# Kernel tuning notes

Hardware: AMD Instinct MI355X
Metric: run time of the kernel (lower is better)

Reference implementation:

```python
import jax, jax.numpy as jnp
import numpy as np

NQ = 100000   # query-side nodes (len of `input`)
NKV = 100000  # key/value-side nodes (len of `other`)
E = 2000000   # edges
D = 64        # n_embed
H = 4         # n_heads
F = D // H    # head dim


def setup_inputs() -> dict:
    key = jax.random.key(0)
    ks = jax.random.split(key, 8)
    sc = 1.0 / np.sqrt(D).astype(np.float32)
    inp = jax.random.normal(ks[0], (NQ, D), jnp.float32)
    oth = jax.random.normal(ks[1], (NKV, D), jnp.float32)
    t = jax.random.randint(ks[2], (E,), 0, NQ, jnp.int32)
    s = jax.random.randint(ks[3], (E,), 0, NKV, jnp.int32)
    Wq = jax.random.normal(ks[4], (D, D), jnp.float32) * sc    # p_q weight (applied as x @ Wq)
    Wkv = jax.random.normal(ks[5], (D, 2 * D), jnp.float32) * sc  # p_kv weight
    Wo = jax.random.normal(ks[6], (D, D), jnp.float32) * sc    # out weight
    bo = jax.random.normal(ks[7], (D,), jnp.float32) * sc      # out bias
    return {"input": inp, "other": oth, "t": t, "s": s,
            "Wq": Wq, "Wkv": Wkv, "Wo": Wo, "bo": bo}


def reference(input, other, t, s, Wq, Wkv, Wo, bo):
    # projections: q [NQ,H,F], k/v [NKV,H,F]
    q = (input @ Wq).reshape(NQ, H, F)
    kv = other @ Wkv
    k = kv[:, :D].reshape(NKV, H, F)
    v = kv[:, D:].reshape(NKV, H, F)

    # per-edge attention scores: [E, H]
    score = jnp.einsum('ehf,ehf->eh', q[t], k[s]) / jnp.sqrt(jnp.float32(F))

    # scatter-softmax over edges grouped by target node t (dim_size = NQ)
    smax = jax.ops.segment_max(score, t, num_segments=NQ)          # [NQ, H]
    smax = jnp.where(jnp.isfinite(smax), smax, jnp.float32(0.0))   # empty segments
    ex = jnp.exp(score - smax[t])                                  # [E, H]
    ssum = jax.ops.segment_sum(ex, t, num_segments=NQ)             # [NQ, H]
    alpha = ex / ssum[t]                                           # [E, H]

    # scatter-sum of weighted values: [NQ, H, F]
    out = jax.ops.segment_sum(alpha[..., None] * v[s], t, num_segments=NQ)
    return out.reshape(NQ, D) @ Wo + bo
```

## Files before the change

kernel.cpp:

```cpp
#include <hip/hip_runtime.h>
#include <math.h>

#define NQn 100000
#define NKVn 100000
#define NEn 2000000

__global__ void zero_kernel(float4* __restrict__ p, int n4) {
    int i = blockIdx.x * blockDim.x + threadIdx.x;
    int stride = gridDim.x * blockDim.x;
    for (; i < n4; i += stride) p[i] = make_float4(0.f, 0.f, 0.f, 0.f);
}

template<int NC>
__global__ void proj_kernel(const float* __restrict__ x, const float* __restrict__ W,
                            float* __restrict__ out, int nrows) {
    __shared__ float Wl[64 * NC];
    for (int i = threadIdx.x; i < 64 * NC; i += blockDim.x) Wl[i] = W[i];
    __syncthreads();
    const int lane = threadIdx.x & 63;
    const int wid  = blockIdx.x * (blockDim.x >> 6) + (threadIdx.x >> 6);
    const int nw   = gridDim.x * (blockDim.x >> 6);
    for (int r = wid; r < nrows; r += nw) {
        float xv = x[(size_t)r * 64 + lane];
        float acc0 = 0.f, acc1 = 0.f;
        #pragma unroll
        for (int k = 0; k < 64; ++k) {
            float xk = __shfl(xv, k, 64);
            acc0 += xk * Wl[k * NC + lane];
            if (NC == 128) acc1 += xk * Wl[k * NC + lane + 64];
        }
        out[(size_t)r * NC + lane] = acc0;
        if (NC == 128) out[(size_t)r * NC + lane + 64] = acc1;
    }
}

__global__ void edge_kernel(const int* __restrict__ t, const int* __restrict__ s,
                            const float* __restrict__ q, const float* __restrict__ kvb,
                            float* __restrict__ acc, float* __restrict__ ssum) {
    const int lane = threadIdx.x & 63;
    const int wid  = blockIdx.x * (blockDim.x >> 6) + (threadIdx.x >> 6);
    const int nw   = gridDim.x * (blockDim.x >> 6);
    for (int e = wid; e < NEn; e += nw) {
        int ti = t[e], si = s[e];
        float qv = q[(size_t)ti * 64 + lane];
        float kk = kvb[(size_t)si * 128 + lane];
        float p = qv * kk;
        p += __shfl_xor(p, 8, 64);
        p += __shfl_xor(p, 4, 64);
        p += __shfl_xor(p, 2, 64);
        p += __shfl_xor(p, 1, 64);
        float ex = __expf(p * 0.25f);
        float vv = kvb[(size_t)si * 128 + 64 + lane];
        atomicAdd(&acc[(size_t)ti * 64 + lane], ex * vv);
        if ((lane & 15) == 0) atomicAdd(&ssum[(size_t)ti * 4 + (lane >> 4)], ex);
    }
}

__global__ void out_kernel(const float* __restrict__ acc, const float* __restrict__ ssum,
                           const float* __restrict__ Wo, const float* __restrict__ bo,
                           float* __restrict__ out) {
    __shared__ float Wl[64 * 64];
    for (int i = threadIdx.x; i < 64 * 64; i += blockDim.x) Wl[i] = Wo[i];
    __syncthreads();
    const int lane = threadIdx.x & 63;
    const int wid  = blockIdx.x * (blockDim.x >> 6) + (threadIdx.x >> 6);
    const int nw   = gridDim.x * (blockDim.x >> 6);
    const float b = bo[lane];
    for (int r = wid; r < NQn; r += nw) {
        float a  = acc[(size_t)r * 64 + lane];
        float su = ssum[(size_t)r * 4 + (lane >> 4)];
        float val = (su > 0.f) ? a / su : 0.f;
        float o = b;
        #pragma unroll
        for (int k = 0; k < 64; ++k)
            o += __shfl(val, k, 64) * Wl[k * 64 + lane];
        out[(size_t)r * 64 + lane] = o;
    }
}

extern "C" void kernel_launch(void* const* d_in, const int* in_sizes, int n_in,
                              void* d_out, int out_size, void* d_ws, size_t ws_size,
                              hipStream_t stream) {
    const float* input = (const float*)d_in[0];
    const float* other = (const float*)d_in[1];
    const int*   t     = (const int*)  d_in[2];
    const int*   s     = (const int*)  d_in[3];
    const float* Wq    = (const float*)d_in[4];
    const float* Wkv   = (const float*)d_in[5];
    const float* Wo    = (const float*)d_in[6];
    const float* bo    = (const float*)d_in[7];
    float* out = (float*)d_out;

    float* ws   = (float*)d_ws;
    float* q    = ws;
    float* kvb  = q   + (size_t)NQn * 64;
    float* acc  = kvb + (size_t)NKVn * 128;
    float* ssum = acc + (size_t)NQn * 64;

    int n4 = (NQn * 64 + NQn * 4) / 4;
    zero_kernel<<<2048, 256, 0, stream>>>((float4*)acc, n4);

    proj_kernel<64> <<<1024, 256, 0, stream>>>(input, Wq,  q,   NQn);
    proj_kernel<128><<<1024, 256, 0, stream>>>(other, Wkv, kvb, NKVn);
    edge_kernel     <<<4096, 256, 0, stream>>>(t, s, q, kvb, acc, ssum);
    out_kernel      <<<1024, 256, 0, stream>>>(acc, ssum, Wo, bo, out);
}
```

Measured before the change: 898.7 us.

## Build CSR by target node and aggregate edges per node without atomics

```diff
diff --git a/kernel.cpp b/kernel.cpp
--- a/kernel.cpp
+++ b/kernel.cpp
@@ -4,76 +4,156 @@
 #define NQn 100000
 #define NKVn 100000
 #define NEn 2000000
+#define SCAN_NB ((NQn + 1023) / 1024)
 
-__global__ void zero_kernel(float4* __restrict__ p, int n4) {
+__global__ void zero_kernel(int* __restrict__ p, int n) {
     int i = blockIdx.x * blockDim.x + threadIdx.x;
     int stride = gridDim.x * blockDim.x;
-    for (; i < n4; i += stride) p[i] = make_float4(0.f, 0.f, 0.f, 0.f);
+    for (; i < n; i += stride) p[i] = 0;
 }
 
-template<int NC>
-__global__ void proj_kernel(const float* __restrict__ x, const float* __restrict__ W,
-                            float* __restrict__ out, int nrows) {
-    __shared__ float Wl[64 * NC];
-    for (int i = threadIdx.x; i < 64 * NC; i += blockDim.x) Wl[i] = W[i];
+__global__ void hist_kernel(const int* __restrict__ t, int* __restrict__ cnt) {
+    int i = blockIdx.x * blockDim.x + threadIdx.x;
+    int stride = gridDim.x * blockDim.x;
+    for (; i < NEn; i += stride) atomicAdd(&cnt[t[i]], 1);
+}
+
+__global__ void scan_bsum_kernel(const int* __restrict__ cnt, int* __restrict__ bsum) {
+    __shared__ int ls[256];
+    int b = blockIdx.x;
+    int base = b * 1024 + threadIdx.x * 4;
+    int tot = 0;
+    #pragma unroll
+    for (int k = 0; k < 4; ++k) {
+        int idx = base + k;
+        tot += (idx < NQn) ? cnt[idx] : 0;
+    }
+    ls[threadIdx.x] = tot;
+    __syncthreads();
+    for (int off = 128; off > 0; off >>= 1) {
+        if (threadIdx.x < off) ls[threadIdx.x] += ls[threadIdx.x + off];
+        __syncthreads();
+    }
+    if (threadIdx.x == 0) bsum[b] = ls[0];
+}
+
+__global__ void scan_base_kernel(const int* __restrict__ bsum, int* __restrict__ bbase,
+                                 int* __restrict__ ptr) {
+    if (threadIdx.x == 0 && blockIdx.x == 0) {
+        int run = 0;
+        for (int b = 0; b < SCAN_NB; ++b) { bbase[b] = run; run += bsum[b]; }
+        ptr[NQn] = run;
+    }
+}
+
+__global__ void scan_final_kernel(const int* __restrict__ cnt, const int* __restrict__ bbase,
+                                  int* __restrict__ ptr, int* __restrict__ fill) {
+    __shared__ int ls[256];
+    int b = blockIdx.x;
+    int base = b * 1024 + threadIdx.x * 4;
+    int c[4];
+    int tot = 0;
+    #pragma unroll
+    for (int k = 0; k < 4; ++k) {
+        int idx = base + k;
+        c[k] = (idx < NQn) ? cnt[idx] : 0;
+        tot += c[k];
+    }
+    ls[threadIdx.x] = tot;
+    __syncthreads();
+    for (int off = 1; off < 256; off <<= 1) {
+        int v = (threadIdx.x >= off) ? ls[threadIdx.x - off] : 0;
+        __syncthreads();
+        ls[threadIdx.x] += v;
+        __syncthreads();
+    }
+    int run = ((threadIdx.x > 0) ? ls[threadIdx.x - 1] : 0) + bbase[b];
+    #pragma unroll
+    for (int k = 0; k < 4; ++k) {
+        int idx = base + k;
+        if (idx < NQn) { ptr[idx] = run; fill[idx] = run; run += c[k]; }
+    }
+}
+
+__global__ void scatter_kernel(const int* __restrict__ t, const int* __restrict__ s,
+                               int* __restrict__ fill, int* __restrict__ sorted_s) {
+    int i = blockIdx.x * blockDim.x + threadIdx.x;
+    int stride = gridDim.x * blockDim.x;
+    for (; i < NEn; i += stride) {
+        int pos = atomicAdd(&fill[t[i]], 1);
+        sorted_s[pos] = s[i];
+    }
+}
+
+__global__ void kvproj_kernel(const float* __restrict__ x, const float* __restrict__ W,
+                              float* __restrict__ out) {
+    __shared__ float Wl[64 * 128];
+    for (int i = threadIdx.x; i < 64 * 128; i += blockDim.x) Wl[i] = W[i];
     __syncthreads();
     const int lane = threadIdx.x & 63;
     const int wid  = blockIdx.x * (blockDim.x >> 6) + (threadIdx.x >> 6);
     const int nw   = gridDim.x * (blockDim.x >> 6);
-    for (int r = wid; r < nrows; r += nw) {
+    for (int r = wid; r < NKVn; r += nw) {
         float xv = x[(size_t)r * 64 + lane];
         float acc0 = 0.f, acc1 = 0.f;
         #pragma unroll
         for (int k = 0; k < 64; ++k) {
             float xk = __shfl(xv, k, 64);
-            acc0 += xk * Wl[k * NC + lane];
-            if (NC == 128) acc1 += xk * Wl[k * NC + lane + 64];
+            acc0 += xk * Wl[k * 128 + lane];
+            acc1 += xk * Wl[k * 128 + lane + 64];
         }
-        out[(size_t)r * NC + lane] = acc0;
-        if (NC == 128) out[(size_t)r * NC + lane + 64] = acc1;
+        out[(size_t)r * 128 + lane]      = acc0;
+        out[(size_t)r * 128 + lane + 64] = acc1;
     }
 }
 
-__global__ void edge_kernel(const int* __restrict__ t, const int* __restrict__ s,
-                            const float* __restrict__ q, const float* __restrict__ kvb,
-                            float* __restrict__ acc, float* __restrict__ ssum) {
-    const int lane = threadIdx.x & 63;
-    const int wid  = blockIdx.x * (blockDim.x >> 6) + (threadIdx.x >> 6);
-    const int nw   = gridDim.x * (blockDim.x >> 6);
-    for (int e = wid; e < NEn; e += nw) {
-        int ti = t[e], si = s[e];
-        float qv = q[(size_t)ti * 64 + lane];
-        float kk = kvb[(size_t)si * 128 + lane];
-        float p = qv * kk;
-        p += __shfl_xor(p, 8, 64);
-        p += __shfl_xor(p, 4, 64);
-        p += __shfl_xor(p, 2, 64);
-        p += __shfl_xor(p, 1, 64);
-        float ex = __expf(p * 0.25f);
-        float vv = kvb[(size_t)si * 128 + 64 + lane];
-        atomicAdd(&acc[(size_t)ti * 64 + lane], ex * vv);
-        if ((lane & 15) == 0) atomicAdd(&ssum[(size_t)ti * 4 + (lane >> 4)], ex);
+__global__ void node_kernel(const float* __restrict__ input, const float* __restrict__ Wq,
+                            const int* __restrict__ ptr, const int* __restrict__ sorted_s,
+                            const float* __restrict__ kvb,
+                            const float* __restrict__ Wo, const float* __restrict__ bo,
+                            float* __restrict__ out) {
+    __shared__ float WqL[64 * 64];
+    __shared__ float WoL[64 * 64];
+    for (int i = threadIdx.x; i < 64 * 64; i += blockDim.x) {
+        WqL[i] = Wq[i];
+        WoL[i] = Wo[i];
     }
-}
-
-__global__ void out_kernel(const float* __restrict__ acc, const float* __restrict__ ssum,
-                           const float* __restrict__ Wo, const float* __restrict__ bo,
-                           float* __restrict__ out) {
-    __shared__ float Wl[64 * 64];
-    for (int i = threadIdx.x; i < 64 * 64; i += blockDim.x) Wl[i] = Wo[i];
     __syncthreads();
     const int lane = threadIdx.x & 63;
     const int wid  = blockIdx.x * (blockDim.x >> 6) + (threadIdx.x >> 6);
     const int nw   = gridDim.x * (blockDim.x >> 6);
     const float b = bo[lane];
+
     for (int r = wid; r < NQn; r += nw) {
-        float a  = acc[(size_t)r * 64 + lane];
-        float su = ssum[(size_t)r * 4 + (lane >> 4)];
-        float val = (su > 0.f) ? a / su : 0.f;
+        float xv = input[(size_t)r * 64 + lane];
+        float qv = 0.f;
+        #pragma unroll
+        for (int k = 0; k < 64; ++k)
+            qv += __shfl(xv, k, 64) * WqL[k * 64 + lane];
+
+        int beg = ptr[r], end = ptr[r + 1];
+        float accl = 0.f, sl = 0.f;
+        int si_next = (beg < end) ? sorted_s[beg] : 0;
+        for (int e = beg; e < end; ++e) {
+            int si = si_next;
+            if (e + 1 < end) si_next = sorted_s[e + 1];
+            float kk = kvb[(size_t)si * 128 + lane];
+            float vv = kvb[(size_t)si * 128 + 64 + lane];
+            float p = qv * kk;
+            p += __shfl_xor(p, 8, 64);
+            p += __shfl_xor(p, 4, 64);
+            p += __shfl_xor(p, 2, 64);
+            p += __shfl_xor(p, 1, 64);
+            float ex = __expf(p * 0.25f);
+            accl += ex * vv;
+            sl   += ex;
+        }
+        float val = (end > beg) ? accl / sl : 0.f;
+
         float o = b;
         #pragma unroll
         for (int k = 0; k < 64; ++k)
-            o += __shfl(val, k, 64) * Wl[k * 64 + lane];
+            o += __shfl(val, k, 64) * WoL[k * 64 + lane];
         out[(size_t)r * 64 + lane] = o;
     }
 }
@@ -91,17 +171,22 @@
     const float* bo    = (const float*)d_in[7];
     float* out = (float*)d_out;
 
-    float* ws   = (float*)d_ws;
-    float* q    = ws;
-    float* kvb  = q   + (size_t)NQn * 64;
-    float* acc  = kvb + (size_t)NKVn * 128;
-    float* ssum = acc + (size_t)NQn * 64;
+    char* w = (char*)d_ws;
+    float* kvb      = (float*)w;                 w += (size_t)NKVn * 128 * 4;
+    int*   cnt      = (int*)w;                   w += (size_t)NQn * 4;
+    int*   ptr      = (int*)w;                   w += ((size_t)NQn + 1) * 4;
+    int*   fill     = (int*)w;                   w += (size_t)NQn * 4;
+    int*   sorted_s = (int*)w;                   w += (size_t)NEn * 4;
+    int*   bsum     = (int*)w;                   w += (size_t)SCAN_NB * 4;
+    int*   bbase    = (int*)w;
 
-    int n4 = (NQn * 64 + NQn * 4) / 4;
-    zero_kernel<<<2048, 256, 0, stream>>>((float4*)acc, n4);
+    zero_kernel   <<<256, 256, 0, stream>>>(cnt, NQn);
+    hist_kernel   <<<2048, 256, 0, stream>>>(t, cnt);
+    scan_bsum_kernel <<<SCAN_NB, 256, 0, stream>>>(cnt, bsum);
+    scan_base_kernel <<<1, 64, 0, stream>>>(bsum, bbase, ptr);
+    scan_final_kernel<<<SCAN_NB, 256, 0, stream>>>(cnt, bbase, ptr, fill);
+    scatter_kernel<<<2048, 256, 0, stream>>>(t, s, fill, sorted_s);
 
-    proj_kernel<64> <<<1024, 256, 0, stream>>>(input, Wq,  q,   NQn);
-    proj_kernel<128><<<1024, 256, 0, stream>>>(other, Wkv, kvb, NKVn);
-    edge_kernel     <<<4096, 256, 0, stream>>>(t, s, q, kvb, acc, ssum);
-    out_kernel      <<<1024, 256, 0, stream>>>(acc, ssum, Wo, bo, out);
+    kvproj_kernel <<<1024, 256, 0, stream>>>(other, Wkv, kvb);
+    node_kernel   <<<4096, 256, 0, stream>>>(input, Wq, ptr, sorted_s, kvb, Wo, bo, out);
 }
```

After: 1.567 ms. 1.74x slower.
